# Kernel tuning notes

Hardware: AMD Instinct MI355X
Metric: run time of the kernel (lower is better)

The kernel has to match this reference:

```python
import jax, jax.numpy as jnp
import numpy as np

N = 100000      # nodes
E = 1600000     # edges
F_IN = 256      # input feature dim
H = 2           # num heads
D = 64          # hidden per head (H*D = 128)
C = 64          # output classes
N_TRAIN = 10000
SLOPE = 0.2     # DGL GATConv leaky_relu negative slope
BN_EPS = 1e-5


def setup_inputs() -> dict:
    key = jax.random.key(0)
    ks = jax.random.split(key, 20)
    sc = lambda k, shape, fan: jax.random.normal(k, shape, jnp.float32) * np.float32(1.0 / np.sqrt(fan))
    inp = {}
    inp["feature"] = jax.random.normal(ks[0], (N, F_IN), jnp.float32)
    inp["label"] = jax.random.randint(ks[1], (N,), 0, C, dtype=jnp.int32)
    inp["train_nodes"] = jax.random.randint(ks[2], (N_TRAIN,), 0, N, dtype=jnp.int32)
    inp["src"] = jax.random.randint(ks[3], (E,), 0, N, dtype=jnp.int32)
    inp["dst"] = jax.random.randint(ks[4], (E,), 0, N, dtype=jnp.int32)
    # GATConv layer 0: F_IN -> H*D
    inp["W0"] = sc(ks[5], (F_IN, H * D), F_IN)
    inp["al0"] = sc(ks[6], (H, D), D)
    inp["ar0"] = sc(ks[7], (H, D), D)
    inp["b0"] = jnp.zeros((H * D,), jnp.float32)
    # GATConv layer 1: H*D -> H*D
    inp["W1"] = sc(ks[8], (H * D, H * D), H * D)
    inp["al1"] = sc(ks[9], (H, D), D)
    inp["ar1"] = sc(ks[10], (H, D), D)
    inp["b1"] = jnp.zeros((H * D,), jnp.float32)
    # dense head: Linear(H*D -> D) + ReLU, Linear(D -> C), BatchNorm1d(C)
    inp["Wout"] = sc(ks[11], (H * D, D), H * D)
    inp["bout"] = jnp.zeros((D,), jnp.float32)
    inp["Wfc"] = sc(ks[12], (D, C), D)
    inp["bfc"] = jnp.zeros((C,), jnp.float32)
    inp["gamma"] = jnp.ones((C,), jnp.float32)
    inp["beta"] = jnp.zeros((C,), jnp.float32)
    return inp


def gat_conv(x, W, al, ar, b, src, dst):
    """DGL-style GATConv: gather, edge attention, segment softmax over dst, scatter-sum, ReLU."""
    n = x.shape[0]
    feat = (x @ W).reshape(n, H, D)                      # [N,H,D]
    el = jnp.einsum('nhd,hd->nh', feat, al)              # src attention term
    er = jnp.einsum('nhd,hd->nh', feat, ar)              # dst attention term
    e = jax.nn.leaky_relu(el[src] + er[dst], SLOPE)      # [E,H]
    m = jax.ops.segment_max(e, dst, num_segments=n)      # per-dst max for stable softmax
    exp_e = jnp.exp(e - m[dst])
    denom = jax.ops.segment_sum(exp_e, dst, num_segments=n)
    alpha = exp_e / jnp.maximum(denom[dst], 1e-16)       # [E,H]
    msg = feat[src] * alpha[:, :, None]                  # [E,H,D]
    out = jax.ops.segment_sum(msg, dst, num_segments=n)  # [N,H,D]
    out = out + b.reshape(1, H, D)
    return jax.nn.relu(out)


def reference(feature, label, train_nodes, src, dst,
              W0, al0, ar0, b0, W1, al1, ar1, b1,
              Wout, bout, Wfc, bfc, gamma, beta):
    h = gat_conv(feature, W0, al0, ar0, b0, src, dst).reshape(N, H * D)
    h = gat_conv(h, W1, al1, ar1, b1, src, dst).reshape(N, H * D)
    h = jax.nn.relu(h @ Wout + bout)
    h = h @ Wfc + bfc
    # BatchNorm1d in training mode: batch statistics (biased variance)
    mu = jnp.mean(h, axis=0)
    var = jnp.mean((h - mu) ** 2, axis=0)
    h = (h - mu) * jax.lax.rsqrt(var + BN_EPS) * gamma + beta
    p = jax.nn.softmax(h, axis=1)
    # F.cross_entropy applied to softmax outputs, exactly as in the source
    sel = p[train_nodes]                                  # [N_TRAIN, C]
    logp = jax.nn.log_softmax(sel, axis=1)
    lab = label[train_nodes]
    loss = -jnp.mean(jnp.take_along_axis(logp, lab[:, None], axis=1))
    return (p, loss)
```

## Files before the change

### kernel.cpp

```cpp
#include <hip/hip_runtime.h>

#define SLOPE 0.2f
#define BN_EPS 1e-5f

#define CSR_TILE 4096
#define NBUCK_SH 9
#define BCAP 16384

typedef __attribute__((ext_vector_type(8))) short bf16x8;
typedef __attribute__((ext_vector_type(4))) float f32x4;

__device__ __forceinline__ float wave_sum(float v){
  #pragma unroll
  for(int o=32;o;o>>=1) v += __shfl_xor(v,o);
  return v;
}
__device__ __forceinline__ float wave_max(float v){
  #pragma unroll
  for(int o=32;o;o>>=1) v = fmaxf(v,__shfl_xor(v,o));
  return v;
}
__device__ __forceinline__ unsigned pack_bf16(float a, float b){
  unsigned ua=__float_as_uint(a), ub=__float_as_uint(b);
  ua += 0x7fffu + ((ua>>16)&1u);
  ub += 0x7fffu + ((ub>>16)&1u);
  return (ua>>16) | (ub & 0xffff0000u);
}
__device__ __forceinline__ float bf_lo(unsigned u){ return __uint_as_float(u<<16); }
__device__ __forceinline__ float bf_hi(unsigned u){ return __uint_as_float(u & 0xffff0000u); }

__global__ __launch_bounds__(256) void wtrans2(const float* __restrict__ W0,
    const float* __restrict__ W1, unsigned* __restrict__ Wt0, unsigned* __restrict__ Wt1,
    int* __restrict__ cursor){
  int idx = blockIdx.x*256 + threadIdx.x;
  if(blockIdx.x < 64){
    int c = idx >> 7, kp = idx & 127;
    Wt0[(size_t)c*128 + kp] = pack_bf16(W0[(size_t)(2*kp)*128 + c], W0[(size_t)(2*kp+1)*128 + c]);
  } else {
    int i2 = idx - 64*256;
    int c = i2 >> 6, kp = i2 & 63;
    Wt1[(size_t)c*64 + kp] = pack_bf16(W1[(size_t)(2*kp)*128 + c], W1[(size_t)(2*kp+1)*128 + c]);
    if(blockIdx.x == 95) cursor[threadIdx.x] = 0;
  }
}

template<int AF32, int KK>
__global__ __launch_bounds__(256) void fat_kernel(const void* __restrict__ Aptr,
    const unsigned* __restrict__ Wt, unsigned* __restrict__ outb,
    const float* __restrict__ al, const float* __restrict__ ar,
    float* __restrict__ el, float* __restrict__ er, int n,
    const int* __restrict__ src, const int* __restrict__ dst,
    int* __restrict__ cursor, unsigned* __restrict__ tmp, int E, int nbuck, int ncsr){
  constexpr int K2 = KK >> 1;
  constexpr int KT = KK >> 6;
  __shared__ unsigned smem[6656];
  int t = threadIdx.x;

  if((int)blockIdx.x < ncsr){
    unsigned* eb  = smem;
    short*    ebb = (short*)(smem + 4096);
    int*      hist= (int*)(smem + 6144);
    int*      basel=(int*)(smem + 6400);
    hist[t] = 0;
    __syncthreads();
    int base = blockIdx.x * CSR_TILE;
    int cnt  = min(CSR_TILE, E - base);
    for(int k = t; k < cnt; k += 256){
      int d = dst[base + k];
      int s = src[base + k];
      int b = d >> NBUCK_SH;
      eb[k]  = (unsigned)s | ((unsigned)(d & ((1<<NBUCK_SH)-1)) << 17);
      ebb[k] = (short)b;
      atomicAdd(&hist[b], 1);
    }
    __syncthreads();
    if(t < nbuck && hist[t] > 0)
      basel[t] = atomicAdd(&cursor[t], hist[t]);
    __syncthreads();
    hist[t] = 0;
    __syncthreads();
    for(int k = t; k < cnt; k += 256){
      int b = ebb[k];
      int r = atomicAdd(&hist[b], 1);
      tmp[(size_t)b*BCAP + basel[b] + r] = eb[k];
    }
    return;
  }

  unsigned (*sA)[36] = (unsigned(*)[36])smem;
  int bid = blockIdx.x - ncsr;
  int w = t >> 6, l = t & 63;
  int wr = (w >> 1) * 64, wc = (w & 1) * 64;
  int row0 = bid * 128;

  int srow[4], sslot[4];
  #pragma unroll
  for(int i=0;i<4;i++){ int u4 = t + i*256; srow[i] = u4>>3; sslot[i] = u4&7; }

  uint4 pa[4][2];

  auto load_tile = [&](int kt){
    if(AF32){
      const float* A = (const float*)Aptr;
      #pragma unroll
      for(int i=0;i<4;i++){
        int gr = row0 + srow[i];
        pa[i][0] = make_uint4(0,0,0,0);
        pa[i][1] = make_uint4(0,0,0,0);
        if(gr < n){
          const unsigned* ap = (const unsigned*)(A + (size_t)gr*KK + kt*64 + sslot[i]*8);
          pa[i][0] = *(const uint4*)ap;
          pa[i][1] = *(const uint4*)(ap+4);
        }
      }
    } else {
      const unsigned* A = (const unsigned*)Aptr;
      #pragma unroll
      for(int i=0;i<4;i++){
        int gr = row0 + srow[i];
        pa[i][0] = make_uint4(0,0,0,0);
        if(gr < n) pa[i][0] = *(const uint4*)(A + (size_t)gr*K2 + kt*32 + sslot[i]*4);
      }
    }
  };

  auto store_tile = [&](){
    if(AF32){
      #pragma unroll
      for(int i=0;i<4;i++){
        uint4 v;
        v.x = pack_bf16(__uint_as_float(pa[i][0].x), __uint_as_float(pa[i][0].y));
        v.y = pack_bf16(__uint_as_float(pa[i][0].z), __uint_as_float(pa[i][0].w));
        v.z = pack_bf16(__uint_as_float(pa[i][1].x), __uint_as_float(pa[i][1].y));
        v.w = pack_bf16(__uint_as_float(pa[i][1].z), __uint_as_float(pa[i][1].w));
        *(uint4*)&sA[srow[i]][sslot[i]*4] = v;
      }
    } else {
      #pragma unroll
      for(int i=0;i<4;i++)
        *(uint4*)&sA[srow[i]][sslot[i]*4] = pa[i][0];
    }
  };

  f32x4 zero4 = {0.f,0.f,0.f,0.f};
  f32x4 acc[4][4];
  #pragma unroll
  for(int i=0;i<4;i++)
    #pragma unroll
    for(int j=0;j<4;j++) acc[i][j] = zero4;

  int rl = l & 15;
  load_tile(0);
  #pragma unroll
  for(int kt = 0; kt < KT; ++kt){
    store_tile();
    __syncthreads();
    if(kt+1 < KT) load_tile(kt+1);
    #pragma unroll
    for(int ks=0; ks<2; ++ks){
      int koff = ks*16 + (l>>4)*4;
      bf16x8 a[4], b[4];
      #pragma unroll
      for(int f=0; f<4; f++)
        b[f] = *(const bf16x8*)&Wt[(size_t)(wc + f*16 + rl)*K2 + kt*32 + koff];
      #pragma unroll
      for(int f=0; f<4; f++)
        a[f] = *(const bf16x8*)&sA[wr + f*16 + rl][koff];
      #pragma unroll
      for(int i=0;i<4;i++)
        #pragma unroll
        for(int j=0;j<4;j++)
          acc[i][j] = __builtin_amdgcn_mfma_f32_16x16x32_bf16(a[i], b[j], acc[i][j], 0, 0, 0);
    }
    __syncthreads();
  }

  #pragma unroll
  for(int i=0;i<4;i++){
    #pragma unroll
    for(int j=0;j<4;j++){
      #pragma unroll
      for(int g=0;g<4;g++){
        float v  = acc[i][j][g];
        float vp = __shfl_xor(v, 1);
        if(!(l & 1)){
          unsigned pv = pack_bf16(v, vp);
          int grow = row0 + wr + i*16 + (l>>4)*4 + g;
          int gcol = wc + j*16 + (l&15);
          if(grow < n) outb[(size_t)grow*64 + (gcol>>1)] = pv;
        }
      }
    }
  }

  {
    int h = wc >> 6;
    float alv[4], arv[4];
    #pragma unroll
    for(int j=0;j<4;j++){
      int c = wc + j*16 + (l&15);
      alv[j] = al[c]; arv[j] = ar[c];
    }
    #pragma unroll
    for(int i=0;i<4;i++){
      #pragma unroll
      for(int g=0;g<4;g++){
        float pe = acc[i][0][g]*alv[0] + acc[i][1][g]*alv[1]
                 + acc[i][2][g]*alv[2] + acc[i][3][g]*alv[3];
        float qe = acc[i][0][g]*arv[0] + acc[i][1][g]*arv[1]
                 + acc[i][2][g]*arv[2] + acc[i][3][g]*arv[3];
        #pragma unroll
        for(int o=8;o;o>>=1){ pe += __shfl_xor(pe,o); qe += __shfl_xor(qe,o); }
        if((l & 15) == 0){
          int grow = row0 + wr + i*16 + (l>>4)*4 + g;
          if(grow < n){
            el[(size_t)grow*2 + h] = pe;
            er[(size_t)grow*2 + h] = qe;
          }
        }
      }
    }
  }
}

__global__ __launch_bounds__(512) void csrD(const unsigned* __restrict__ tmp,
    const int* __restrict__ cursor, int* __restrict__ rowptr,
    int* __restrict__ esrc, int N, int E, int nbuck){
  __shared__ int sc[256];
  __shared__ int hist[512];
  __shared__ int ls[512];
  int t = threadIdx.x;
  int b = blockIdx.x;
  if(t < 256) sc[t] = (t < nbuck) ? cursor[t] : 0;
  __syncthreads();
  for(int o=1;o<256;o<<=1){
    int x = (t>=o && t<256) ? sc[t-o] : 0;
    __syncthreads();
    if(t < 256) sc[t] += x;
    __syncthreads();
  }
  __shared__ int s_base, s_cnt;
  if(t == 0){ s_cnt = cursor[b]; s_base = sc[b] - s_cnt; }
  __syncthreads();
  int base = s_base, cnt = s_cnt;
  const unsigned* tp = tmp + (size_t)b*BCAP;
  int n0 = b << NBUCK_SH;
  int nn = min(512, N - n0);
  hist[t] = 0;
  __syncthreads();
  for(int i = t; i < cnt; i += 512)
    atomicAdd(&hist[tp[i] >> 17], 1);
  __syncthreads();
  int v = hist[t];
  ls[t] = v; __syncthreads();
  for(int o=1;o<512;o<<=1){
    int x = (t>=o) ? ls[t-o] : 0;
    __syncthreads();
    ls[t] += x;
    __syncthreads();
  }
  int rp = ls[t] - v;
  if(t < nn) rowptr[n0 + t] = base + rp;
  if(b == nbuck-1 && t == 0) rowptr[N] = E;
  __syncthreads();
  hist[t] = rp;
  __syncthreads();
  for(int i = t; i < cnt; i += 512){
    unsigned v2 = tp[i];
    int dl = v2 >> 17;
    int s  = v2 & 0x1FFFF;
    int r  = atomicAdd(&hist[dl], 1);
    esrc[base + r] = s;
  }
}

__device__ __forceinline__ void agg_chunk(const unsigned* __restrict__ featb,
    int s, unsigned wp, int nval, int lane, int shamt, float& acc0, float& acc1){
  for(int e = 0; e < nval; e += 8){
    unsigned v[8]; float w[8];
    #pragma unroll
    for(int u=0;u<8;u++){
      int se       = __shfl(s,  e+u);
      unsigned wpe = __shfl(wp, e+u);
      w[u] = __uint_as_float((wpe << shamt) & 0xffff0000u);
      v[u] = featb[((unsigned)se << 6) + (unsigned)lane];
    }
    #pragma unroll
    for(int u=0;u<8;u++){
      acc0 += bf_lo(v[u]) * w[u];
      acc1 += bf_hi(v[u]) * w[u];
    }
  }
}

__global__ __launch_bounds__(256) void agg_kernel(const unsigned* __restrict__ featb,
    const float* __restrict__ el, const float* __restrict__ er,
    const int* __restrict__ rowptr, const int* __restrict__ esrc,
    const float* __restrict__ bias, unsigned* __restrict__ outp, int n){
  int wid = (blockIdx.x*blockDim.x + threadIdx.x) >> 6;
  int lane = threadIdx.x & 63;
  if(wid >= n) return;
  int beg = rowptr[wid], end = rowptr[wid+1];
  int deg = end - beg;
  float2 erd = *(const float2*)&er[(size_t)wid*2];
  int shamt = (lane < 32) ? 16 : 0;
  float acc0 = 0.f, acc1 = 0.f;

  if(deg <= 64){
    int s = (lane < deg) ? esrc[beg + lane] : 0;
    float2 elv = *(const float2*)&el[(size_t)s*2];
    float e0 = elv.x + erd.x, e1 = elv.y + erd.y;
    e0 = (e0 >= 0.f) ? e0 : SLOPE*e0;
    e1 = (e1 >= 0.f) ? e1 : SLOPE*e1;
    float p0 = __expf(e0), p1 = __expf(e1);
    if(lane >= deg){ p0 = 0.f; p1 = 0.f; }
    float d0 = wave_sum(p0), d1 = wave_sum(p1);
    unsigned wp = pack_bf16(p0 / fmaxf(d0, 1e-16f), p1 / fmaxf(d1, 1e-16f));
    agg_chunk(featb, s, wp, deg, lane, shamt, acc0, acc1);
  } else {
    float d0 = 0.f, d1 = 0.f;
    for(int base = beg; base < end; base += 64){
      int idx = base + lane;
      int s = (idx < end) ? esrc[idx] : 0;
      float2 elv = *(const float2*)&el[(size_t)s*2];
      float e0 = elv.x + erd.x, e1 = elv.y + erd.y;
      e0 = (e0 >= 0.f) ? e0 : SLOPE*e0;
      e1 = (e1 >= 0.f) ? e1 : SLOPE*e1;
      float p0 = __expf(e0), p1 = __expf(e1);
      if(idx >= end){ p0 = 0.f; p1 = 0.f; }
      d0 += p0; d1 += p1;
    }
    d0 = wave_sum(d0); d1 = wave_sum(d1);
    float inv0 = 1.0f / fmaxf(d0, 1e-16f);
    float inv1 = 1.0f / fmaxf(d1, 1e-16f);
    for(int base = beg; base < end; base += 64){
      int idx = base + lane;
      int s = (idx < end) ? esrc[idx] : 0;
      float2 elv = *(const float2*)&el[(size_t)s*2];
      float e0 = elv.x + erd.x, e1 = elv.y + erd.y;
      e0 = (e0 >= 0.f) ? e0 : SLOPE*e0;
      e1 = (e1 >= 0.f) ? e1 : SLOPE*e1;
      unsigned wp = pack_bf16(__expf(e0) * inv0, __expf(e1) * inv1);
      if(idx >= end) wp = 0;
      agg_chunk(featb, s, wp, min(64, end - base), lane, shamt, acc0, acc1);
    }
  }
  float2 bb = *(const float2*)&bias[2*lane];
  outp[(size_t)wid*64 + lane] =
      pack_bf16(fmaxf(acc0 + bb.x, 0.f), fmaxf(acc1 + bb.y, 0.f));
}

__global__ __launch_bounds__(256) void head_kernel(const unsigned* __restrict__ h,
    const float* __restrict__ Wout, const float* __restrict__ bout,
    const float* __restrict__ Wfc, const float* __restrict__ bfc,
    float* __restrict__ hfc, float* __restrict__ psum, float* __restrict__ psum2,
    int n){
  __shared__ float sAT[32][68];
  __shared__ float sWo[32][68];
  __shared__ float sOT[64][68];
  __shared__ float sF [64][68];
  int t = threadIdx.x;
  int cx = t & 15;
  int ry = t >> 4;
  int row0 = blockIdx.x * 64;

  {
    int kr = t >> 4;
    int c0 = (t & 15) * 4;
    #pragma unroll
    for(int i=0;i<4;i++)
      *(float4*)&sF[kr+i*16][c0] = *(const float4*)&Wfc[(size_t)(kr+i*16)*64 + c0];
  }

  float acc[4][4] = {};
  for(int k0 = 0; k0 < 128; k0 += 32){
    #pragma unroll
    for(int u=0;u<2;u++){
      int f4 = t*2 + u;
      int r  = f4 >> 3;
      int kc = (f4 & 7) * 4;
      int gr = row0 + r;
      uint2 v = make_uint2(0,0);
      if(gr < n) v = *(const uint2*)&h[(size_t)gr*64 + ((k0+kc)>>1)];
      sAT[kc+0][r] = bf_lo(v.x);
      sAT[kc+1][r] = bf_hi(v.x);
      sAT[kc+2][r] = bf_lo(v.y);
      sAT[kc+3][r] = bf_hi(v.y);
    }
    #pragma unroll
    for(int u=0;u<2;u++){
      int f4 = t*2 + u;
      int kr = f4 >> 4;
      int c0 = (f4 & 15) * 4;
      *(float4*)&sWo[kr][c0] = *(const float4*)&Wout[(size_t)(k0+kr)*64 + c0];
    }
    __syncthreads();
    #pragma unroll 8
    for(int kk = 0; kk < 32; ++kk){
      float4 a4 = *(const float4*)&sAT[kk][ry*4];
      float4 b4 = *(const float4*)&sWo[kk][cx*4];
      float a[4] = {a4.x,a4.y,a4.z,a4.w};
      float b[4] = {b4.x,b4.y,b4.z,b4.w};
      #pragma unroll
      for(int i=0;i<4;i++)
        #pragma unroll
        for(int j=0;j<4;j++) acc[i][j] += a[i]*b[j];
    }
    __syncthreads();
  }
  {
    float4 bb = *(const float4*)&bout[cx*4];
    float bv[4] = {bb.x,bb.y,bb.z,bb.w};
    #pragma unroll
    for(int i=0;i<4;i++)
      #pragma unroll
      for(int j=0;j<4;j++)
        sOT[cx*4+j][ry*4+i] = fmaxf(acc[i][j] + bv[j], 0.f);
  }
  __syncthreads();
  float acc2[4][4] = {};
  #pragma unroll 8
  for(int kk = 0; kk < 64; ++kk){
    float4 a4 = *(const float4*)&sOT[kk][ry*4];
    float4 b4 = *(const float4*)&sF [kk][cx*4];
    float a[4] = {a4.x,a4.y,a4.z,a4.w};
    float b[4] = {b4.x,b4.y,b4.z,b4.w};
    #pragma unroll
    for(int i=0;i<4;i++)
      #pragma unroll
      for(int j=0;j<4;j++) acc2[i][j] += a[i]*b[j];
  }
  __syncthreads();
  {
    float4 bb = *(const float4*)&bfc[cx*4];
    float bv[4] = {bb.x,bb.y,bb.z,bb.w};
    #pragma unroll
    for(int i=0;i<4;i++){
      int gr = row0 + ry*4 + i;
      float o0 = acc2[i][0]+bv[0], o1 = acc2[i][1]+bv[1];
      float o2 = acc2[i][2]+bv[2], o3 = acc2[i][3]+bv[3];
      if(gr < n){
        *(float4*)&hfc[(size_t)gr*64 + cx*4] = make_float4(o0,o1,o2,o3);
        sOT[ry*4+i][cx*4+0] = o0;
        sOT[ry*4+i][cx*4+1] = o1;
        sOT[ry*4+i][cx*4+2] = o2;
        sOT[ry*4+i][cx*4+3] = o3;
      } else {
        sOT[ry*4+i][cx*4+0] = 0.f;
        sOT[ry*4+i][cx*4+1] = 0.f;
        sOT[ry*4+i][cx*4+2] = 0.f;
        sOT[ry*4+i][cx*4+3] = 0.f;
      }
    }
  }
  __syncthreads();
  if(t < 64){
    float s = 0.f, s2 = 0.f;
    #pragma unroll 8
    for(int r = 0; r < 64; ++r){
      float v = sOT[r][t];
      s += v; s2 += v*v;
    }
    psum [(size_t)blockIdx.x*64 + t] = s;
    psum2[(size_t)blockIdx.x*64 + t] = s2;
  }
}

__global__ __launch_bounds__(256) void bn_red(const float* __restrict__ psum,
    const float* __restrict__ psum2, float* __restrict__ rsum,
    float* __restrict__ rsum2, int nb){
  __shared__ float ls[256], ls2[256];
  int t = threadIdx.x; int c = t & 63; int g = t >> 6;
  int R = (nb + 127) / 128;
  int r0 = blockIdx.x * R;
  int r1 = min(nb, r0 + R);
  float s = 0.f, s2 = 0.f;
  for(int r = r0 + g; r < r1; r += 4){
    s  += psum [(size_t)r*64 + c];
    s2 += psum2[(size_t)r*64 + c];
  }
  ls[t] = s; ls2[t] = s2;
  __syncthreads();
  if(t < 64){
    rsum [(size_t)blockIdx.x*64 + t] = ls[t]+ls[t+64]+ls[t+128]+ls[t+192];
    rsum2[(size_t)blockIdx.x*64 + t] = ls2[t]+ls2[t+64]+ls2[t+128]+ls2[t+192];
  }
}

__global__ __launch_bounds__(256) void bn_fin(const float* __restrict__ rsum,
    const float* __restrict__ rsum2, const float* __restrict__ gamma,
    const float* __restrict__ beta, float* __restrict__ scsh, int n){
  __shared__ float ls[256], ls2[256];
  int t = threadIdx.x; int c = t & 63; int g = t >> 6;
  float s = 0.f, s2 = 0.f;
  for(int b = g; b < 128; b += 4){
    s  += rsum [(size_t)b*64 + c];
    s2 += rsum2[(size_t)b*64 + c];
  }
  ls[t] = s; ls2[t] = s2;
  __syncthreads();
  if(t < 64){
    s  = ls[t]+ls[t+64]+ls[t+128]+ls[t+192];
    s2 = ls2[t]+ls2[t+64]+ls2[t+128]+ls2[t+192];
    float mu  = s / n;
    float var = s2 / n - mu*mu;
    float scale = rsqrtf(var + BN_EPS) * gamma[t];
    scsh[t]    = scale;
    scsh[64+t] = beta[t] - mu*scale;
  }
}

__global__ __launch_bounds__(256) void bn_softmax(const float* __restrict__ hfc,
    const float* __restrict__ scsh, float* __restrict__ p, int n){
  int wid = (blockIdx.x*blockDim.x + threadIdx.x) >> 6;
  int lane = threadIdx.x & 63;
  if(wid >= n) return;
  float y = hfc[(size_t)wid*64 + lane]*scsh[lane] + scsh[64+lane];
  float m = wave_max(y);
  float e = expf(y - m);
  float s = wave_sum(e);
  p[(size_t)wid*64 + lane] = e / s;
}

__global__ __launch_bounds__(256) void loss1(const float* __restrict__ p,
    const int* __restrict__ train, const int* __restrict__ label,
    float* __restrict__ part, int ntrain){
  int lane = threadIdx.x & 63; int w = threadIdx.x >> 6;
  int gw = blockIdx.x*4 + w; int nw = gridDim.x*4;
  float acc = 0.f;
  for(int t = gw; t < ntrain; t += nw){
    int node = train[t];
    float v = p[(size_t)node*64 + lane];
    float m = wave_max(v);
    float e = expf(v - m);
    float s = wave_sum(e);
    float logp = (v - m) - logf(s);
    int lab = label[node];
    if(lane == lab) acc += logp;
  }
  acc = wave_sum(acc);
  __shared__ float ls[4];
  if(lane == 0) ls[w] = acc;
  __syncthreads();
  if(threadIdx.x == 0) part[blockIdx.x] = ls[0]+ls[1]+ls[2]+ls[3];
}

__global__ void loss2(const float* __restrict__ part, float* __restrict__ out,
                      int nb, int ntrain){
  if(threadIdx.x == 0){
    float s = 0.f;
    for(int i=0;i<nb;i++) s += part[i];
    out[0] = -s / (float)ntrain;
  }
}

extern "C" void kernel_launch(void* const* d_in, const int* in_sizes, int n_in,
                              void* d_out, int out_size, void* d_ws, size_t ws_size,
                              hipStream_t stream){
  const float* feature = (const float*)d_in[0];
  const int*   label   = (const int*)d_in[1];
  const int*   train   = (const int*)d_in[2];
  const int*   src     = (const int*)d_in[3];
  const int*   dst     = (const int*)d_in[4];
  const float* W0   = (const float*)d_in[5];
  const float* al0  = (const float*)d_in[6];
  const float* ar0  = (const float*)d_in[7];
  const float* b0   = (const float*)d_in[8];
  const float* W1   = (const float*)d_in[9];
  const float* al1  = (const float*)d_in[10];
  const float* ar1  = (const float*)d_in[11];
  const float* b1   = (const float*)d_in[12];
  const float* Wout = (const float*)d_in[13];
  const float* bout = (const float*)d_in[14];
  const float* Wfc  = (const float*)d_in[15];
  const float* bfc  = (const float*)d_in[16];
  const float* gamma= (const float*)d_in[17];
  const float* beta = (const float*)d_in[18];

  const int N  = in_sizes[1];
  const int NT = in_sizes[2];
  const int E  = in_sizes[3];

  const int nbuck  = (N + (1<<NBUCK_SH) - 1) >> NBUCK_SH;
  const int ntiles = (E + CSR_TILE - 1) / CSR_TILE;
  const int ngemm  = (N + 127) / 128;
  const int nhead  = (N + 63) / 64;

  size_t off = 0;
  auto alloc = [&](size_t bytes)->void*{
    void* pp = (char*)d_ws + off;
    off += (bytes + 255) & ~(size_t)255;
    return pp;
  };
  unsigned* featb16 = (unsigned*)alloc((size_t)N*64*4);
  unsigned* hbuf2   = (unsigned*)alloc((size_t)N*64*4);
  float* el      = (float*)alloc((size_t)N*2*4);
  float* er      = (float*)alloc((size_t)N*2*4);
  int*   rowptr  = (int*)alloc((size_t)(N+1)*4);
  int*   esrc    = (int*)alloc((size_t)E*4);
  int*   cursor  = (int*)alloc((size_t)256*4);
  unsigned* Wt0  = (unsigned*)alloc((size_t)128*128*4);
  unsigned* Wt1  = (unsigned*)alloc((size_t)128*64*4);
  float* psum    = (float*)alloc((size_t)(nhead+1)*64*4);
  float* psum2   = (float*)alloc((size_t)(nhead+1)*64*4);
  float* rsum    = (float*)alloc((size_t)128*64*4);
  float* rsum2   = (float*)alloc((size_t)128*64*4);
  float* scsh    = (float*)alloc(128*4);
  float* lpart   = (float*)alloc(256*4);
  float* hfc     = (float*)featb16;
  unsigned* tmp  = hbuf2;

  float* p_out   = (float*)d_out;
  float* loss_out= (float*)d_out + (size_t)N*64;

  const int nwaveblk = (N + 3) / 4;

  wtrans2<<<96, 256, 0, stream>>>(W0, W1, Wt0, Wt1, cursor);

  fat_kernel<1,256><<<ntiles + ngemm, 256, 0, stream>>>(feature, Wt0, featb16,
      al0, ar0, el, er, N, src, dst, cursor, tmp, E, nbuck, ntiles);

  csrD<<<nbuck, 512, 0, stream>>>(tmp, cursor, rowptr, esrc, N, E, nbuck);

  agg_kernel<<<nwaveblk, 256, 0, stream>>>(featb16, el, er, rowptr, esrc, b0, hbuf2, N);

  fat_kernel<0,128><<<ngemm, 256, 0, stream>>>(hbuf2, Wt1, featb16,
      al1, ar1, el, er, N, src, dst, cursor, tmp, E, nbuck, 0);

  agg_kernel<<<nwaveblk, 256, 0, stream>>>(featb16, el, er, rowptr, esrc, b1, hbuf2, N);

  head_kernel<<<nhead, 256, 0, stream>>>(hbuf2, Wout, bout, Wfc, bfc, hfc, psum, psum2, N);

  bn_red<<<128, 256, 0, stream>>>(psum, psum2, rsum, rsum2, nhead);
  bn_fin<<<1, 256, 0, stream>>>(rsum, rsum2, gamma, beta, scsh, N);

  bn_softmax<<<nwaveblk, 256, 0, stream>>>(hfc, scsh, p_out, N);

  loss1<<<40, 256, 0, stream>>>(p_out, train, label, lpart, NT);
  loss2<<<1, 64, 0, stream>>>(lpart, loss_out, 40, NT);
}
```

Before: 366.3 us.

## Fuse layer-0 aggregation with layer-1 GEMM into one kernel

Adds an agg_gemm kernel in which each block aggregates 128 destination nodes into shared memory, one wave per node. It then runs the layer-1 bf16 MFMA GEMM and the attention projections directly from that tile. This removes the global write and re-read of the layer-0 output and one kernel launch. The cost is that the GEMM now runs at occupancy limited by the larger shared tile. Buffers are reassigned and separate el/er arrays are used for each layer to avoid read/write overlap.

After: 464.5 us. 1.27x slower.

```diff
diff --git a/kernel.cpp b/kernel.cpp
--- a/kernel.cpp
+++ b/kernel.cpp
@@ -29,251 +29,6 @@
 __device__ __forceinline__ float bf_lo(unsigned u){ return __uint_as_float(u<<16); }
 __device__ __forceinline__ float bf_hi(unsigned u){ return __uint_as_float(u & 0xffff0000u); }
 
-__global__ __launch_bounds__(256) void wtrans2(const float* __restrict__ W0,
-    const float* __restrict__ W1, unsigned* __restrict__ Wt0, unsigned* __restrict__ Wt1,
-    int* __restrict__ cursor){
-  int idx = blockIdx.x*256 + threadIdx.x;
-  if(blockIdx.x < 64){
-    int c = idx >> 7, kp = idx & 127;
-    Wt0[(size_t)c*128 + kp] = pack_bf16(W0[(size_t)(2*kp)*128 + c], W0[(size_t)(2*kp+1)*128 + c]);
-  } else {
-    int i2 = idx - 64*256;
-    int c = i2 >> 6, kp = i2 & 63;
-    Wt1[(size_t)c*64 + kp] = pack_bf16(W1[(size_t)(2*kp)*128 + c], W1[(size_t)(2*kp+1)*128 + c]);
-    if(blockIdx.x == 95) cursor[threadIdx.x] = 0;
-  }
-}
-
-template<int AF32, int KK>
-__global__ __launch_bounds__(256) void fat_kernel(const void* __restrict__ Aptr,
-    const unsigned* __restrict__ Wt, unsigned* __restrict__ outb,
-    const float* __restrict__ al, const float* __restrict__ ar,
-    float* __restrict__ el, float* __restrict__ er, int n,
-    const int* __restrict__ src, const int* __restrict__ dst,
-    int* __restrict__ cursor, unsigned* __restrict__ tmp, int E, int nbuck, int ncsr){
-  constexpr int K2 = KK >> 1;
-  constexpr int KT = KK >> 6;
-  __shared__ unsigned smem[6656];
-  int t = threadIdx.x;
-
-  if((int)blockIdx.x < ncsr){
-    unsigned* eb  = smem;
-    short*    ebb = (short*)(smem + 4096);
-    int*      hist= (int*)(smem + 6144);
-    int*      basel=(int*)(smem + 6400);
-    hist[t] = 0;
-    __syncthreads();
-    int base = blockIdx.x * CSR_TILE;
-    int cnt  = min(CSR_TILE, E - base);
-    for(int k = t; k < cnt; k += 256){
-      int d = dst[base + k];
-      int s = src[base + k];
-      int b = d >> NBUCK_SH;
-      eb[k]  = (unsigned)s | ((unsigned)(d & ((1<<NBUCK_SH)-1)) << 17);
-      ebb[k] = (short)b;
-      atomicAdd(&hist[b], 1);
-    }
-    __syncthreads();
-    if(t < nbuck && hist[t] > 0)
-      basel[t] = atomicAdd(&cursor[t], hist[t]);
-    __syncthreads();
-    hist[t] = 0;
-    __syncthreads();
-    for(int k = t; k < cnt; k += 256){
-      int b = ebb[k];
-      int r = atomicAdd(&hist[b], 1);
-      tmp[(size_t)b*BCAP + basel[b] + r] = eb[k];
-    }
-    return;
-  }
-
-  unsigned (*sA)[36] = (unsigned(*)[36])smem;
-  int bid = blockIdx.x - ncsr;
-  int w = t >> 6, l = t & 63;
-  int wr = (w >> 1) * 64, wc = (w & 1) * 64;
-  int row0 = bid * 128;
-
-  int srow[4], sslot[4];
-  #pragma unroll
-  for(int i=0;i<4;i++){ int u4 = t + i*256; srow[i] = u4>>3; sslot[i] = u4&7; }
-
-  uint4 pa[4][2];
-
-  auto load_tile = [&](int kt){
-    if(AF32){
-      const float* A = (const float*)Aptr;
-      #pragma unroll
-      for(int i=0;i<4;i++){
-        int gr = row0 + srow[i];
-        pa[i][0] = make_uint4(0,0,0,0);
-        pa[i][1] = make_uint4(0,0,0,0);
-        if(gr < n){
-          const unsigned* ap = (const unsigned*)(A + (size_t)gr*KK + kt*64 + sslot[i]*8);
-          pa[i][0] = *(const uint4*)ap;
-          pa[i][1] = *(const uint4*)(ap+4);
-        }
-      }
-    } else {
-      const unsigned* A = (const unsigned*)Aptr;
-      #pragma unroll
-      for(int i=0;i<4;i++){
-        int gr = row0 + srow[i];
-        pa[i][0] = make_uint4(0,0,0,0);
-        if(gr < n) pa[i][0] = *(const uint4*)(A + (size_t)gr*K2 + kt*32 + sslot[i]*4);
-      }
-    }
-  };
-
-  auto store_tile = [&](){
-    if(AF32){
-      #pragma unroll
-      for(int i=0;i<4;i++){
-        uint4 v;
-        v.x = pack_bf16(__uint_as_float(pa[i][0].x), __uint_as_float(pa[i][0].y));
-        v.y = pack_bf16(__uint_as_float(pa[i][0].z), __uint_as_float(pa[i][0].w));
-        v.z = pack_bf16(__uint_as_float(pa[i][1].x), __uint_as_float(pa[i][1].y));
-        v.w = pack_bf16(__uint_as_float(pa[i][1].z), __uint_as_float(pa[i][1].w));
-        *(uint4*)&sA[srow[i]][sslot[i]*4] = v;
-      }
-    } else {
-      #pragma unroll
-      for(int i=0;i<4;i++)
-        *(uint4*)&sA[srow[i]][sslot[i]*4] = pa[i][0];
-    }
-  };
-
-  f32x4 zero4 = {0.f,0.f,0.f,0.f};
-  f32x4 acc[4][4];
-  #pragma unroll
-  for(int i=0;i<4;i++)
-    #pragma unroll
-    for(int j=0;j<4;j++) acc[i][j] = zero4;
-
-  int rl = l & 15;
-  load_tile(0);
-  #pragma unroll
-  for(int kt = 0; kt < KT; ++kt){
-    store_tile();
-    __syncthreads();
-    if(kt+1 < KT) load_tile(kt+1);
-    #pragma unroll
-    for(int ks=0; ks<2; ++ks){
-      int koff = ks*16 + (l>>4)*4;
-      bf16x8 a[4], b[4];
-      #pragma unroll
-      for(int f=0; f<4; f++)
-        b[f] = *(const bf16x8*)&Wt[(size_t)(wc + f*16 + rl)*K2 + kt*32 + koff];
-      #pragma unroll
-      for(int f=0; f<4; f++)
-        a[f] = *(const bf16x8*)&sA[wr + f*16 + rl][koff];
-      #pragma unroll
-      for(int i=0;i<4;i++)
-        #pragma unroll
-        for(int j=0;j<4;j++)
-          acc[i][j] = __builtin_amdgcn_mfma_f32_16x16x32_bf16(a[i], b[j], acc[i][j], 0, 0, 0);
-    }
-    __syncthreads();
-  }
-
-  #pragma unroll
-  for(int i=0;i<4;i++){
-    #pragma unroll
-    for(int j=0;j<4;j++){
-      #pragma unroll
-      for(int g=0;g<4;g++){
-        float v  = acc[i][j][g];
-        float vp = __shfl_xor(v, 1);
-        if(!(l & 1)){
-          unsigned pv = pack_bf16(v, vp);
-          int grow = row0 + wr + i*16 + (l>>4)*4 + g;
-          int gcol = wc + j*16 + (l&15);
-          if(grow < n) outb[(size_t)grow*64 + (gcol>>1)] = pv;
-        }
-      }
-    }
-  }
-
-  {
-    int h = wc >> 6;
-    float alv[4], arv[4];
-    #pragma unroll
-    for(int j=0;j<4;j++){
-      int c = wc + j*16 + (l&15);
-      alv[j] = al[c]; arv[j] = ar[c];
-    }
-    #pragma unroll
-    for(int i=0;i<4;i++){
-      #pragma unroll
-      for(int g=0;g<4;g++){
-        float pe = acc[i][0][g]*alv[0] + acc[i][1][g]*alv[1]
-                 + acc[i][2][g]*alv[2] + acc[i][3][g]*alv[3];
-        float qe = acc[i][0][g]*arv[0] + acc[i][1][g]*arv[1]
-                 + acc[i][2][g]*arv[2] + acc[i][3][g]*arv[3];
-        #pragma unroll
-        for(int o=8;o;o>>=1){ pe += __shfl_xor(pe,o); qe += __shfl_xor(qe,o); }
-        if((l & 15) == 0){
-          int grow = row0 + wr + i*16 + (l>>4)*4 + g;
-          if(grow < n){
-            el[(size_t)grow*2 + h] = pe;
-            er[(size_t)grow*2 + h] = qe;
-          }
-        }
-      }
-    }
-  }
-}
-
-__global__ __launch_bounds__(512) void csrD(const unsigned* __restrict__ tmp,
-    const int* __restrict__ cursor, int* __restrict__ rowptr,
-    int* __restrict__ esrc, int N, int E, int nbuck){
-  __shared__ int sc[256];
-  __shared__ int hist[512];
-  __shared__ int ls[512];
-  int t = threadIdx.x;
-  int b = blockIdx.x;
-  if(t < 256) sc[t] = (t < nbuck) ? cursor[t] : 0;
-  __syncthreads();
-  for(int o=1;o<256;o<<=1){
-    int x = (t>=o && t<256) ? sc[t-o] : 0;
-    __syncthreads();
-    if(t < 256) sc[t] += x;
-    __syncthreads();
-  }
-  __shared__ int s_base, s_cnt;
-  if(t == 0){ s_cnt = cursor[b]; s_base = sc[b] - s_cnt; }
-  __syncthreads();
-  int base = s_base, cnt = s_cnt;
-  const unsigned* tp = tmp + (size_t)b*BCAP;
-  int n0 = b << NBUCK_SH;
-  int nn = min(512, N - n0);
-  hist[t] = 0;
-  __syncthreads();
-  for(int i = t; i < cnt; i += 512)
-    atomicAdd(&hist[tp[i] >> 17], 1);
-  __syncthreads();
-  int v = hist[t];
-  ls[t] = v; __syncthreads();
-  for(int o=1;o<512;o<<=1){
-    int x = (t>=o) ? ls[t-o] : 0;
-    __syncthreads();
-    ls[t] += x;
-    __syncthreads();
-  }
-  int rp = ls[t] - v;
-  if(t < nn) rowptr[n0 + t] = base + rp;
-  if(b == nbuck-1 && t == 0) rowptr[N] = E;
-  __syncthreads();
-  hist[t] = rp;
-  __syncthreads();
-  for(int i = t; i < cnt; i += 512){
-    unsigned v2 = tp[i];
-    int dl = v2 >> 17;
-    int s  = v2 & 0x1FFFF;
-    int r  = atomicAdd(&hist[dl], 1);
-    esrc[base + r] = s;
-  }
-}
-
 __device__ __forceinline__ void agg_chunk(const unsigned* __restrict__ featb,
     int s, unsigned wp, int nval, int lane, int shamt, float& acc0, float& acc1){
   for(int e = 0; e < nval; e += 8){
@@ -293,13 +48,10 @@
   }
 }
 
-__global__ __launch_bounds__(256) void agg_kernel(const unsigned* __restrict__ featb,
+__device__ __forceinline__ unsigned agg_node(const unsigned* __restrict__ featb,
     const float* __restrict__ el, const float* __restrict__ er,
     const int* __restrict__ rowptr, const int* __restrict__ esrc,
-    const float* __restrict__ bias, unsigned* __restrict__ outp, int n){
-  int wid = (blockIdx.x*blockDim.x + threadIdx.x) >> 6;
-  int lane = threadIdx.x & 63;
-  if(wid >= n) return;
+    const float* __restrict__ bias, int wid, int lane){
   int beg = rowptr[wid], end = rowptr[wid+1];
   int deg = end - beg;
   float2 erd = *(const float2*)&er[(size_t)wid*2];
@@ -346,8 +98,337 @@
     }
   }
   float2 bb = *(const float2*)&bias[2*lane];
-  outp[(size_t)wid*64 + lane] =
-      pack_bf16(fmaxf(acc0 + bb.x, 0.f), fmaxf(acc1 + bb.y, 0.f));
+  return pack_bf16(fmaxf(acc0 + bb.x, 0.f), fmaxf(acc1 + bb.y, 0.f));
+}
+
+__global__ __launch_bounds__(256) void wtrans2(const float* __restrict__ W0,
+    const float* __restrict__ W1, unsigned* __restrict__ Wt0, unsigned* __restrict__ Wt1,
+    int* __restrict__ cursor){
+  int idx = blockIdx.x*256 + threadIdx.x;
+  if(blockIdx.x < 64){
+    int c = idx >> 7, kp = idx & 127;
+    Wt0[(size_t)c*128 + kp] = pack_bf16(W0[(size_t)(2*kp)*128 + c], W0[(size_t)(2*kp+1)*128 + c]);
+  } else {
+    int i2 = idx - 64*256;
+    int c = i2 >> 6, kp = i2 & 63;
+    Wt1[(size_t)c*64 + kp] = pack_bf16(W1[(size_t)(2*kp)*128 + c], W1[(size_t)(2*kp+1)*128 + c]);
+    if(blockIdx.x == 95) cursor[threadIdx.x] = 0;
+  }
+}
+
+__global__ __launch_bounds__(256) void fat_kernel0(const float* __restrict__ A,
+    const unsigned* __restrict__ Wt, unsigned* __restrict__ outb,
+    const float* __restrict__ al, const float* __restrict__ ar,
+    float* __restrict__ el, float* __restrict__ er, int n,
+    const int* __restrict__ src, const int* __restrict__ dst,
+    int* __restrict__ cursor, unsigned* __restrict__ tmp, int E, int nbuck, int ncsr){
+  constexpr int KK = 256, K2 = 128, KT = 4;
+  __shared__ unsigned smem[6656];
+  int t = threadIdx.x;
+
+  if((int)blockIdx.x < ncsr){
+    unsigned* eb  = smem;
+    short*    ebb = (short*)(smem + 4096);
+    int*      hist= (int*)(smem + 6144);
+    int*      basel=(int*)(smem + 6400);
+    hist[t] = 0;
+    __syncthreads();
+    int base = blockIdx.x * CSR_TILE;
+    int cnt  = min(CSR_TILE, E - base);
+    for(int k = t; k < cnt; k += 256){
+      int d = dst[base + k];
+      int s = src[base + k];
+      int b = d >> NBUCK_SH;
+      eb[k]  = (unsigned)s | ((unsigned)(d & ((1<<NBUCK_SH)-1)) << 17);
+      ebb[k] = (short)b;
+      atomicAdd(&hist[b], 1);
+    }
+    __syncthreads();
+    if(t < nbuck && hist[t] > 0)
+      basel[t] = atomicAdd(&cursor[t], hist[t]);
+    __syncthreads();
+    hist[t] = 0;
+    __syncthreads();
+    for(int k = t; k < cnt; k += 256){
+      int b = ebb[k];
+      int r = atomicAdd(&hist[b], 1);
+      tmp[(size_t)b*BCAP + basel[b] + r] = eb[k];
+    }
+    return;
+  }
+
+  unsigned (*sA)[36] = (unsigned(*)[36])smem;
+  int bid = blockIdx.x - ncsr;
+  int w = t >> 6, l = t & 63;
+  int wr = (w >> 1) * 64, wc = (w & 1) * 64;
+  int row0 = bid * 128;
+
+  int srow[4], sslot[4];
+  #pragma unroll
+  for(int i=0;i<4;i++){ int u4 = t + i*256; srow[i] = u4>>3; sslot[i] = u4&7; }
+
+  uint4 pa[4][2];
+
+  auto load_tile = [&](int kt){
+    #pragma unroll
+    for(int i=0;i<4;i++){
+      int gr = row0 + srow[i];
+      pa[i][0] = make_uint4(0,0,0,0);
+      pa[i][1] = make_uint4(0,0,0,0);
+      if(gr < n){
+        const unsigned* ap = (const unsigned*)(A + (size_t)gr*KK + kt*64 + sslot[i]*8);
+        pa[i][0] = *(const uint4*)ap;
+        pa[i][1] = *(const uint4*)(ap+4);
+      }
+    }
+  };
+  auto store_tile = [&](){
+    #pragma unroll
+    for(int i=0;i<4;i++){
+      uint4 v;
+      v.x = pack_bf16(__uint_as_float(pa[i][0].x), __uint_as_float(pa[i][0].y));
+      v.y = pack_bf16(__uint_as_float(pa[i][0].z), __uint_as_float(pa[i][0].w));
+      v.z = pack_bf16(__uint_as_float(pa[i][1].x), __uint_as_float(pa[i][1].y));
+      v.w = pack_bf16(__uint_as_float(pa[i][1].z), __uint_as_float(pa[i][1].w));
+      *(uint4*)&sA[srow[i]][sslot[i]*4] = v;
+    }
+  };
+
+  f32x4 zero4 = {0.f,0.f,0.f,0.f};
+  f32x4 acc[4][4];
+  #pragma unroll
+  for(int i=0;i<4;i++)
+    #pragma unroll
+    for(int j=0;j<4;j++) acc[i][j] = zero4;
+
+  int rl = l & 15;
+  load_tile(0);
+  #pragma unroll
+  for(int kt = 0; kt < KT; ++kt){
+    store_tile();
+    __syncthreads();
+    if(kt+1 < KT) load_tile(kt+1);
+    #pragma unroll
+    for(int ks=0; ks<2; ++ks){
+      int koff = ks*16 + (l>>4)*4;
+      bf16x8 a[4], b[4];
+      #pragma unroll
+      for(int f=0; f<4; f++)
+        b[f] = *(const bf16x8*)&Wt[(size_t)(wc + f*16 + rl)*K2 + kt*32 + koff];
+      #pragma unroll
+      for(int f=0; f<4; f++)
+        a[f] = *(const bf16x8*)&sA[wr + f*16 + rl][koff];
+      #pragma unroll
+      for(int i=0;i<4;i++)
+        #pragma unroll
+        for(int j=0;j<4;j++)
+          acc[i][j] = __builtin_amdgcn_mfma_f32_16x16x32_bf16(a[i], b[j], acc[i][j], 0, 0, 0);
+    }
+    __syncthreads();
+  }
+
+  #pragma unroll
+  for(int i=0;i<4;i++){
+    #pragma unroll
+    for(int j=0;j<4;j++){
+      #pragma unroll
+      for(int g=0;g<4;g++){
+        float v  = acc[i][j][g];
+        float vp = __shfl_xor(v, 1);
+        if(!(l & 1)){
+          unsigned pv = pack_bf16(v, vp);
+          int grow = row0 + wr + i*16 + (l>>4)*4 + g;
+          int gcol = wc + j*16 + (l&15);
+          if(grow < n) outb[(size_t)grow*64 + (gcol>>1)] = pv;
+        }
+      }
+    }
+  }
+  {
+    int h = wc >> 6;
+    float alv[4], arv[4];
+    #pragma unroll
+    for(int j=0;j<4;j++){
+      int c = wc + j*16 + (l&15);
+      alv[j] = al[c]; arv[j] = ar[c];
+    }
+    #pragma unroll
+    for(int i=0;i<4;i++){
+      #pragma unroll
+      for(int g=0;g<4;g++){
+        float pe = acc[i][0][g]*alv[0] + acc[i][1][g]*alv[1]
+                 + acc[i][2][g]*alv[2] + acc[i][3][g]*alv[3];
+        float qe = acc[i][0][g]*arv[0] + acc[i][1][g]*arv[1]
+                 + acc[i][2][g]*arv[2] + acc[i][3][g]*arv[3];
+        #pragma unroll
+        for(int o=8;o;o>>=1){ pe += __shfl_xor(pe,o); qe += __shfl_xor(qe,o); }
+        if((l & 15) == 0){
+          int grow = row0 + wr + i*16 + (l>>4)*4 + g;
+          if(grow < n){
+            el[(size_t)grow*2 + h] = pe;
+            er[(size_t)grow*2 + h] = qe;
+          }
+        }
+      }
+    }
+  }
+}
+
+__global__ __launch_bounds__(256) void agg_gemm(const unsigned* __restrict__ featb,
+    const float* __restrict__ el0, const float* __restrict__ er0,
+    const int* __restrict__ rowptr, const int* __restrict__ esrc,
+    const float* __restrict__ bias, const unsigned* __restrict__ Wt,
+    unsigned* __restrict__ outb, const float* __restrict__ al,
+    const float* __restrict__ ar, float* __restrict__ el1,
+    float* __restrict__ er1, int n){
+  __shared__ unsigned sA[128][68];
+  int t = threadIdx.x;
+  int w = t >> 6, l = t & 63;
+  int row0 = blockIdx.x * 128;
+
+  for(int r = w; r < 128; r += 4){
+    int node = row0 + r;
+    unsigned u = 0;
+    if(node < n) u = agg_node(featb, el0, er0, rowptr, esrc, bias, node, l);
+    sA[r][l] = u;
+  }
+  __syncthreads();
+
+  int wr = (w >> 1) * 64, wc = (w & 1) * 64;
+  int rl = l & 15;
+  f32x4 zero4 = {0.f,0.f,0.f,0.f};
+  f32x4 acc[4][4];
+  #pragma unroll
+  for(int i=0;i<4;i++)
+    #pragma unroll
+    for(int j=0;j<4;j++) acc[i][j] = zero4;
+
+  #pragma unroll
+  for(int kt = 0; kt < 2; ++kt){
+    #pragma unroll
+    for(int ks=0; ks<2; ++ks){
+      int koff = kt*32 + ks*16 + (l>>4)*4;
+      bf16x8 a[4], b[4];
+      #pragma unroll
+      for(int f=0; f<4; f++)
+        b[f] = *(const bf16x8*)&Wt[(size_t)(wc + f*16 + rl)*64 + koff];
+      #pragma unroll
+      for(int f=0; f<4; f++)
+        a[f] = *(const bf16x8*)&sA[wr + f*16 + rl][koff];
+      #pragma unroll
+      for(int i=0;i<4;i++)
+        #pragma unroll
+        for(int j=0;j<4;j++)
+          acc[i][j] = __builtin_amdgcn_mfma_f32_16x16x32_bf16(a[i], b[j], acc[i][j], 0, 0, 0);
+    }
+  }
+
+  #pragma unroll
+  for(int i=0;i<4;i++){
+    #pragma unroll
+    for(int j=0;j<4;j++){
+      #pragma unroll
+      for(int g=0;g<4;g++){
+        float v  = acc[i][j][g];
+        float vp = __shfl_xor(v, 1);
+        if(!(l & 1)){
+          unsigned pv = pack_bf16(v, vp);
+          int grow = row0 + wr + i*16 + (l>>4)*4 + g;
+          int gcol = wc + j*16 + (l&15);
+          if(grow < n) outb[(size_t)grow*64 + (gcol>>1)] = pv;
+        }
+      }
+    }
+  }
+  {
+    int h = wc >> 6;
+    float alv[4], arv[4];
+    #pragma unroll
+    for(int j=0;j<4;j++){
+      int c = wc + j*16 + (l&15);
+      alv[j] = al[c]; arv[j] = ar[c];
+    }
+    #pragma unroll
+    for(int i=0;i<4;i++){
+      #pragma unroll
+      for(int g=0;g<4;g++){
+        float pe = acc[i][0][g]*alv[0] + acc[i][1][g]*alv[1]
+                 + acc[i][2][g]*alv[2] + acc[i][3][g]*alv[3];
+        float qe = acc[i][0][g]*arv[0] + acc[i][1][g]*arv[1]
+                 + acc[i][2][g]*arv[2] + acc[i][3][g]*arv[3];
+        #pragma unroll
+        for(int o=8;o;o>>=1){ pe += __shfl_xor(pe,o); qe += __shfl_xor(qe,o); }
+        if((l & 15) == 0){
+          int grow = row0 + wr + i*16 + (l>>4)*4 + g;
+          if(grow < n){
+            el1[(size_t)grow*2 + h] = pe;
+            er1[(size_t)grow*2 + h] = qe;
+          }
+        }
+      }
+    }
+  }
+}
+
+__global__ __launch_bounds__(512) void csrD(const unsigned* __restrict__ tmp,
+    const int* __restrict__ cursor, int* __restrict__ rowptr,
+    int* __restrict__ esrc, int N, int E, int nbuck){
+  __shared__ int sc[256];
+  __shared__ int hist[512];
+  __shared__ int ls[512];
+  int t = threadIdx.x;
+  int b = blockIdx.x;
+  if(t < 256) sc[t] = (t < nbuck) ? cursor[t] : 0;
+  __syncthreads();
+  for(int o=1;o<256;o<<=1){
+    int x = (t>=o && t<256) ? sc[t-o] : 0;
+    __syncthreads();
+    if(t < 256) sc[t] += x;
+    __syncthreads();
+  }
+  __shared__ int s_base, s_cnt;
+  if(t == 0){ s_cnt = cursor[b]; s_base = sc[b] - s_cnt; }
+  __syncthreads();
+  int base = s_base, cnt = s_cnt;
+  const unsigned* tp = tmp + (size_t)b*BCAP;
+  int n0 = b << NBUCK_SH;
+  int nn = min(512, N - n0);
+  hist[t] = 0;
+  __syncthreads();
+  for(int i = t; i < cnt; i += 512)
+    atomicAdd(&hist[tp[i] >> 17], 1);
+  __syncthreads();
+  int v = hist[t];
+  ls[t] = v; __syncthreads();
+  for(int o=1;o<512;o<<=1){
+    int x = (t>=o) ? ls[t-o] : 0;
+    __syncthreads();
+    ls[t] += x;
+    __syncthreads();
+  }
+  int rp = ls[t] - v;
+  if(t < nn) rowptr[n0 + t] = base + rp;
+  if(b == nbuck-1 && t == 0) rowptr[N] = E;
+  __syncthreads();
+  hist[t] = rp;
+  __syncthreads();
+  for(int i = t; i < cnt; i += 512){
+    unsigned v2 = tp[i];
+    int dl = v2 >> 17;
+    int s  = v2 & 0x1FFFF;
+    int r  = atomicAdd(&hist[dl], 1);
+    esrc[base + r] = s;
+  }
+}
+
+__global__ __launch_bounds__(256) void agg_kernel(const unsigned* __restrict__ featb,
+    const float* __restrict__ el, const float* __restrict__ er,
+    const int* __restrict__ rowptr, const int* __restrict__ esrc,
+    const float* __restrict__ bias, unsigned* __restrict__ outp, int n){
+  int wid = (blockIdx.x*blockDim.x + threadIdx.x) >> 6;
+  int lane = threadIdx.x & 63;
+  if(wid >= n) return;
+  outp[(size_t)wid*64 + lane] = agg_node(featb, el, er, rowptr, esrc, bias, wid, lane);
 }
 
 __global__ __launch_bounds__(256) void head_kernel(const unsigned* __restrict__ h,
@@ -594,8 +675,10 @@
   };
   unsigned* featb16 = (unsigned*)alloc((size_t)N*64*4);
   unsigned* hbuf2   = (unsigned*)alloc((size_t)N*64*4);
-  float* el      = (float*)alloc((size_t)N*2*4);
-  float* er      = (float*)alloc((size_t)N*2*4);
+  float* el0     = (float*)alloc((size_t)N*2*4);
+  float* er0     = (float*)alloc((size_t)N*2*4);
+  float* el1     = (float*)alloc((size_t)N*2*4);
+  float* er1     = (float*)alloc((size_t)N*2*4);
   int*   rowptr  = (int*)alloc((size_t)(N+1)*4);
   int*   esrc    = (int*)alloc((size_t)E*4);
   int*   cursor  = (int*)alloc((size_t)256*4);
@@ -607,8 +690,8 @@
   float* rsum2   = (float*)alloc((size_t)128*64*4);
   float* scsh    = (float*)alloc(128*4);
   float* lpart   = (float*)alloc(256*4);
-  float* hfc     = (float*)featb16;
   unsigned* tmp  = hbuf2;
+  float* hfc     = (float*)hbuf2;
 
   float* p_out   = (float*)d_out;
   float* loss_out= (float*)d_out + (size_t)N*64;
@@ -617,19 +700,17 @@
 
   wtrans2<<<96, 256, 0, stream>>>(W0, W1, Wt0, Wt1, cursor);
 
-  fat_kernel<1,256><<<ntiles + ngemm, 256, 0, stream>>>(feature, Wt0, featb16,
-      al0, ar0, el, er, N, src, dst, cursor, tmp, E, nbuck, ntiles);
+  fat_kernel0<<<ntiles + ngemm, 256, 0, stream>>>(feature, Wt0, featb16,
+      al0, ar0, el0, er0, N, src, dst, cursor, tmp, E, nbuck, ntiles);
 
   csrD<<<nbuck, 512, 0, stream>>>(tmp, cursor, rowptr, esrc, N, E, nbuck);
 
-  agg_kernel<<<nwaveblk, 256, 0, stream>>>(featb16, el, er, rowptr, esrc, b0, hbuf2, N);
-
-  fat_kernel<0,128><<<ngemm, 256, 0, stream>>>(hbuf2, Wt1, featb16,
-      al1, ar1, el, er, N, src, dst, cursor, tmp, E, nbuck, 0);
-
-  agg_kernel<<<nwaveblk, 256, 0, stream>>>(featb16, el, er, rowptr, esrc, b1, hbuf2, N);
-
-  head_kernel<<<nhead, 256, 0, stream>>>(hbuf2, Wout, bout, Wfc, bfc, hfc, psum, psum2, N);
+  agg_gemm<<<ngemm, 256, 0, stream>>>(featb16, el0, er0, rowptr, esrc, b0,
+      Wt1, hbuf2, al1, ar1, el1, er1, N);
+
+  agg_kernel<<<nwaveblk, 256, 0, stream>>>(hbuf2, el1, er1, rowptr, esrc, b1, featb16, N);
+
+  head_kernel<<<nhead, 256, 0, stream>>>(featb16, Wout, bout, Wfc, bfc, hfc, psum, psum2, N);
 
   bn_red<<<128, 256, 0, stream>>>(psum, psum2, rsum, rsum2, nhead);
   bn_fin<<<1, 256, 0, stream>>>(rsum, rsum2, gamma, beta, scsh, N);
```

## Restructure fused GEMM to per-wave 16-row tiles without shared-memory staging

Applied to the files above, without the earlier changes.

The dense projection GEMM inside the fused kernel switches from a 128x128 block tile staged through LDS with barriers to a layout where each wave computes 16 full-width rows directly from global memory, loading its A fragment into registers. Launch bounds now request 4 blocks per CU, and the grid doubles since each block covers 64 rows. The aim is to remove LDS traffic and syncthreads and to raise occupancy for this memory-bound, skinny GEMM. In exchange, the weight fragments are re-read from global or cache by every wave, and the A loads are less coalesced.

New measurement: 397.9 us. 8.6% more time.

```diff
diff --git a/kernel.cpp b/kernel.cpp
--- a/kernel.cpp
+++ b/kernel.cpp
@@ -45,14 +45,14 @@
 }
 
 template<int AF32, int KK>
-__global__ __launch_bounds__(256) void fat_kernel(const void* __restrict__ Aptr,
+__global__ __launch_bounds__(256, 4) void fat_kernel(const void* __restrict__ Aptr,
     const unsigned* __restrict__ Wt, unsigned* __restrict__ outb,
     const float* __restrict__ al, const float* __restrict__ ar,
     float* __restrict__ el, float* __restrict__ er, int n,
     const int* __restrict__ src, const int* __restrict__ dst,
     int* __restrict__ cursor, unsigned* __restrict__ tmp, int E, int nbuck, int ncsr){
   constexpr int K2 = KK >> 1;
-  constexpr int KT = KK >> 6;
+  constexpr int KS = KK >> 5;
   __shared__ unsigned smem[6656];
   int t = threadIdx.x;
 
@@ -87,136 +87,86 @@
     return;
   }
 
-  unsigned (*sA)[36] = (unsigned(*)[36])smem;
   int bid = blockIdx.x - ncsr;
   int w = t >> 6, l = t & 63;
-  int wr = (w >> 1) * 64, wc = (w & 1) * 64;
-  int row0 = bid * 128;
-
-  int srow[4], sslot[4];
+  int rl = l & 15, kg = l >> 4;
+  int wrow0 = (bid*4 + w) * 16;
+  if(wrow0 >= n) return;
+  int growl = wrow0 + rl;
+  bool rok = growl < n;
+
+  f32x4 zero4 = {0.f,0.f,0.f,0.f};
+  f32x4 acc[8];
   #pragma unroll
-  for(int i=0;i<4;i++){ int u4 = t + i*256; srow[i] = u4>>3; sslot[i] = u4&7; }
-
-  uint4 pa[4][2];
-
-  auto load_tile = [&](int kt){
+  for(int j=0;j<8;j++) acc[j] = zero4;
+
+  #pragma unroll 2
+  for(int kt = 0; kt < KS; ++kt){
+    bf16x8 a;
     if(AF32){
       const float* A = (const float*)Aptr;
-      #pragma unroll
-      for(int i=0;i<4;i++){
-        int gr = row0 + srow[i];
-        pa[i][0] = make_uint4(0,0,0,0);
-        pa[i][1] = make_uint4(0,0,0,0);
-        if(gr < n){
-          const unsigned* ap = (const unsigned*)(A + (size_t)gr*KK + kt*64 + sslot[i]*8);
-          pa[i][0] = *(const uint4*)ap;
-          pa[i][1] = *(const uint4*)(ap+4);
-        }
+      float4 f0 = make_float4(0.f,0.f,0.f,0.f);
+      float4 f1 = make_float4(0.f,0.f,0.f,0.f);
+      if(rok){
+        const float* ap = A + (size_t)growl*KK + kt*32 + kg*8;
+        f0 = *(const float4*)ap;
+        f1 = *(const float4*)(ap+4);
       }
+      uint4 uv;
+      uv.x = pack_bf16(f0.x,f0.y); uv.y = pack_bf16(f0.z,f0.w);
+      uv.z = pack_bf16(f1.x,f1.y); uv.w = pack_bf16(f1.z,f1.w);
+      a = __builtin_bit_cast(bf16x8, uv);
     } else {
       const unsigned* A = (const unsigned*)Aptr;
+      uint4 uv = make_uint4(0,0,0,0);
+      if(rok) uv = *(const uint4*)(A + (size_t)growl*K2 + kt*16 + kg*4);
+      a = __builtin_bit_cast(bf16x8, uv);
+    }
+    #pragma unroll
+    for(int j=0;j<8;j++){
+      bf16x8 b = *(const bf16x8*)&Wt[(size_t)(j*16 + rl)*K2 + kt*16 + kg*4];
+      acc[j] = __builtin_amdgcn_mfma_f32_16x16x32_bf16(a, b, acc[j], 0, 0, 0);
+    }
+  }
+
+  #pragma unroll
+  for(int j=0;j<8;j++){
+    #pragma unroll
+    for(int g=0;g<4;g++){
+      float v  = acc[j][g];
+      float vp = __shfl_xor(v, 1);
+      if(!(l & 1)){
+        unsigned pv = pack_bf16(v, vp);
+        int grow = wrow0 + kg*4 + g;
+        int gcol = j*16 + rl;
+        if(grow < n) outb[(size_t)grow*64 + (gcol>>1)] = pv;
+      }
+    }
+  }
+
+  {
+    float alv[8], arv[8];
+    #pragma unroll
+    for(int j=0;j<8;j++){
+      int c = j*16 + rl;
+      alv[j] = al[c]; arv[j] = ar[c];
+    }
+    #pragma unroll
+    for(int g=0;g<4;g++){
+      float pe0 = acc[0][g]*alv[0] + acc[1][g]*alv[1] + acc[2][g]*alv[2] + acc[3][g]*alv[3];
+      float qe0 = acc[0][g]*arv[0] + acc[1][g]*arv[1] + acc[2][g]*arv[2] + acc[3][g]*arv[3];
+      float pe1 = acc[4][g]*alv[4] + acc[5][g]*alv[5] + acc[6][g]*alv[6] + acc[7][g]*alv[7];
+      float qe1 = acc[4][g]*arv[4] + acc[5][g]*arv[5] + acc[6][g]*arv[6] + acc[7][g]*arv[7];
       #pragma unroll
-      for(int i=0;i<4;i++){
-        int gr = row0 + srow[i];
-        pa[i][0] = make_uint4(0,0,0,0);
-        if(gr < n) pa[i][0] = *(const uint4*)(A + (size_t)gr*K2 + kt*32 + sslot[i]*4);
+      for(int o=8;o;o>>=1){
+        pe0 += __shfl_xor(pe0,o); qe0 += __shfl_xor(qe0,o);
+        pe1 += __shfl_xor(pe1,o); qe1 += __shfl_xor(qe1,o);
       }
-    }
-  };
-
-  auto store_tile = [&](){
-    if(AF32){
-      #pragma unroll
-      for(int i=0;i<4;i++){
-        uint4 v;
-        v.x = pack_bf16(__uint_as_float(pa[i][0].x), __uint_as_float(pa[i][0].y));
-        v.y = pack_bf16(__uint_as_float(pa[i][0].z), __uint_as_float(pa[i][0].w));
-        v.z = pack_bf16(__uint_as_float(pa[i][1].x), __uint_as_float(pa[i][1].y));
-        v.w = pack_bf16(__uint_as_float(pa[i][1].z), __uint_as_float(pa[i][1].w));
-        *(uint4*)&sA[srow[i]][sslot[i]*4] = v;
-      }
-    } else {
-      #pragma unroll
-      for(int i=0;i<4;i++)
-        *(uint4*)&sA[srow[i]][sslot[i]*4] = pa[i][0];
-    }
-  };
-
-  f32x4 zero4 = {0.f,0.f,0.f,0.f};
-  f32x4 acc[4][4];
-  #pragma unroll
-  for(int i=0;i<4;i++)
-    #pragma unroll
-    for(int j=0;j<4;j++) acc[i][j] = zero4;
-
-  int rl = l & 15;
-  load_tile(0);
-  #pragma unroll
-  for(int kt = 0; kt < KT; ++kt){
-    store_tile();
-    __syncthreads();
-    if(kt+1 < KT) load_tile(kt+1);
-    #pragma unroll
-    for(int ks=0; ks<2; ++ks){
-      int koff = ks*16 + (l>>4)*4;
-      bf16x8 a[4], b[4];
-      #pragma unroll
-      for(int f=0; f<4; f++)
-        b[f] = *(const bf16x8*)&Wt[(size_t)(wc + f*16 + rl)*K2 + kt*32 + koff];
-      #pragma unroll
-      for(int f=0; f<4; f++)
-        a[f] = *(const bf16x8*)&sA[wr + f*16 + rl][koff];
-      #pragma unroll
-      for(int i=0;i<4;i++)
-        #pragma unroll
-        for(int j=0;j<4;j++)
-          acc[i][j] = __builtin_amdgcn_mfma_f32_16x16x32_bf16(a[i], b[j], acc[i][j], 0, 0, 0);
-    }
-    __syncthreads();
-  }
-
-  #pragma unroll
-  for(int i=0;i<4;i++){
-    #pragma unroll
-    for(int j=0;j<4;j++){
-      #pragma unroll
-      for(int g=0;g<4;g++){
-        float v  = acc[i][j][g];
-        float vp = __shfl_xor(v, 1);
-        if(!(l & 1)){
-          unsigned pv = pack_bf16(v, vp);
-          int grow = row0 + wr + i*16 + (l>>4)*4 + g;
-          int gcol = wc + j*16 + (l&15);
-          if(grow < n) outb[(size_t)grow*64 + (gcol>>1)] = pv;
-        }
-      }
-    }
-  }
-
-  {
-    int h = wc >> 6;
-    float alv[4], arv[4];
-    #pragma unroll
-    for(int j=0;j<4;j++){
-      int c = wc + j*16 + (l&15);
-      alv[j] = al[c]; arv[j] = ar[c];
-    }
-    #pragma unroll
-    for(int i=0;i<4;i++){
-      #pragma unroll
-      for(int g=0;g<4;g++){
-        float pe = acc[i][0][g]*alv[0] + acc[i][1][g]*alv[1]
-                 + acc[i][2][g]*alv[2] + acc[i][3][g]*alv[3];
-        float qe = acc[i][0][g]*arv[0] + acc[i][1][g]*arv[1]
-                 + acc[i][2][g]*arv[2] + acc[i][3][g]*arv[3];
-        #pragma unroll
-        for(int o=8;o;o>>=1){ pe += __shfl_xor(pe,o); qe += __shfl_xor(qe,o); }
-        if((l & 15) == 0){
-          int grow = row0 + wr + i*16 + (l>>4)*4 + g;
-          if(grow < n){
-            el[(size_t)grow*2 + h] = pe;
-            er[(size_t)grow*2 + h] = qe;
-          }
+      if(rl == 0){
+        int grow = wrow0 + kg*4 + g;
+        if(grow < n){
+          *(float2*)&el[(size_t)grow*2] = make_float2(pe0, pe1);
+          *(float2*)&er[(size_t)grow*2] = make_float2(qe0, qe1);
         }
       }
     }
@@ -583,7 +533,7 @@
 
   const int nbuck  = (N + (1<<NBUCK_SH) - 1) >> NBUCK_SH;
   const int ntiles = (E + CSR_TILE - 1) / CSR_TILE;
-  const int ngemm  = (N + 127) / 128;
+  const int ngemm  = (N + 63) / 64;
   const int nhead  = (N + 63) / 64;
 
   size_t off = 0;
```
